# Performance work log

Measured on AMD Instinct MI355X. Metric: run time of the kernel, lower is better.

The kernel has to match this reference:

```python
import jax, jax.numpy as jnp
import numpy as np

N_NODES = 65536
N_EDGES = 524288
FEAT_DIM = 512
EMBED_DIM = 512


def setup_inputs() -> dict:
    key = jax.random.key(0)
    k1, k2, k3, k4, k5 = jax.random.split(key, 5)
    x = jax.random.normal(k1, (N_NODES, FEAT_DIM), dtype=jnp.float32)
    # xavier_uniform for (embed_dim, feat_dim)
    limit = float(np.sqrt(6.0 / (EMBED_DIM + FEAT_DIM)))
    weight = jax.random.uniform(k2, (EMBED_DIM, FEAT_DIM), dtype=jnp.float32,
                                minval=-limit, maxval=limit)
    row = jax.random.randint(k3, (N_EDGES,), 0, N_NODES, dtype=jnp.int64)
    col = jax.random.randint(k4, (N_EDGES,), 0, N_NODES, dtype=jnp.int64)
    vals = jax.random.uniform(k5, (N_EDGES,), dtype=jnp.float32)
    return {"x": x, "weight": weight, "row": row, "col": col, "vals": vals}


def reference(x, weight, row, col, vals):
    # Fused GEMM + SpMM: out = adj @ (x @ weight.T)
    h = jnp.einsum('nf,ef->ne', x, weight)            # [N, embed_dim] dense GEMM
    msgs = vals[:, None] * h[col]                     # [E, embed_dim] gather + scale
    out = jax.ops.segment_sum(msgs, row, num_segments=N_NODES)  # SpMM scatter-add
    return out
```

## Files before the change

### kernel.cpp

```cpp
#include <hip/hip_runtime.h>
#include <stdint.h>


#define N_NODES 65536
#define N_EDGES 524288
#define FEAT    512
#define EMB     512
#define CAP     64

typedef short  short8  __attribute__((ext_vector_type(8)));
typedef float  floatx4 __attribute__((ext_vector_type(4)));

__device__ __forceinline__ unsigned short f2bf(float f) {
    unsigned int u = __float_as_uint(f);
    u += 0x7FFFu + ((u >> 16) & 1u);
    return (unsigned short)(u >> 16);
}
__device__ __forceinline__ float bf2f_lo(unsigned int u) { return __uint_as_float(u << 16); }
__device__ __forceinline__ float bf2f_hi(unsigned int u) { return __uint_as_float(u & 0xffff0000u); }

#define BM 128
#define BN 64
#define BK 64
#define LDA 72

__global__ __launch_bounds__(256)
void gemm_h(const float* __restrict__ x, const float* __restrict__ w,
            unsigned short* __restrict__ h)
{
    __shared__ unsigned short As[BM][LDA];
    __shared__ unsigned short Bs[BN][LDA];

    const int t    = threadIdx.x;
    const int lane = t & 63;
    const int wave = t >> 6;
    const int wm   = wave >> 1;
    const int wn   = wave & 1;
    const int l15  = lane & 15;
    const int lq   = lane >> 4;

    const int bn = blockIdx.x & 7;
    const int bm = blockIdx.x >> 3;
    const int m0 = bm * BM;
    const int n0 = bn * BN;

    floatx4 acc[4][2];
    #pragma unroll
    for (int i = 0; i < 4; i++)
        #pragma unroll
        for (int j = 0; j < 2; j++)
            acc[i][j] = (floatx4){0.f, 0.f, 0.f, 0.f};

    for (int kb = 0; kb < FEAT; kb += BK) {
        #pragma unroll
        for (int p = 0; p < 8; p++) {
            int idx = p * 256 + t;
            int row = idx >> 4;
            int cv  = (idx & 15) << 2;
            float4 v = *(const float4*)&x[(m0 + row) * FEAT + kb + cv];
            ushort4 b4;
            b4.x = f2bf(v.x); b4.y = f2bf(v.y); b4.z = f2bf(v.z); b4.w = f2bf(v.w);
            *(ushort4*)&As[row][cv] = b4;
        }
        #pragma unroll
        for (int p = 0; p < 4; p++) {
            int idx = p * 256 + t;
            int row = idx >> 4;
            int cv  = (idx & 15) << 2;
            float4 v = *(const float4*)&w[(n0 + row) * FEAT + kb + cv];
            ushort4 b4;
            b4.x = f2bf(v.x); b4.y = f2bf(v.y); b4.z = f2bf(v.z); b4.w = f2bf(v.w);
            *(ushort4*)&Bs[row][cv] = b4;
        }
        __syncthreads();
        #pragma unroll
        for (int kk = 0; kk < 2; kk++) {
            short8 af[4], bfr[2];
            #pragma unroll
            for (int mt = 0; mt < 4; mt++)
                af[mt] = *(const short8*)&As[wm * 64 + mt * 16 + l15][kk * 32 + lq * 8];
            #pragma unroll
            for (int nt = 0; nt < 2; nt++)
                bfr[nt] = *(const short8*)&Bs[wn * 32 + nt * 16 + l15][kk * 32 + lq * 8];
            #pragma unroll
            for (int mt = 0; mt < 4; mt++)
                #pragma unroll
                for (int nt = 0; nt < 2; nt++)
                    acc[mt][nt] = __builtin_amdgcn_mfma_f32_16x16x32_bf16(
                        af[mt], bfr[nt], acc[mt][nt], 0, 0, 0);
        }
        __syncthreads();
    }

    #pragma unroll
    for (int mt = 0; mt < 4; mt++)
        #pragma unroll
        for (int nt = 0; nt < 2; nt++)
            #pragma unroll
            for (int r = 0; r < 4; r++) {
                int row  = m0 + wm * 64 + mt * 16 + lq * 4 + r;
                int colg = n0 + wn * 32 + nt * 16 + l15;
                h[row * EMB + colg] = f2bf(acc[mt][nt][r]);
            }
}

__global__ __launch_bounds__(256)
void fill_edges(const int* __restrict__ row, const int* __restrict__ col,
                const float* __restrict__ vals, int* __restrict__ cnt,
                int* __restrict__ col_s, float* __restrict__ val_s)
{
    int e = blockIdx.x * 256 + threadIdx.x;
    if (e >= N_EDGES) return;
    int r = row[e];
    int slot = atomicAdd(&cnt[r], 1);
    if (slot < CAP) {
        col_s[r * CAP + slot] = col[e];
        val_s[r * CAP + slot] = vals[e];
    }
}

__global__ __launch_bounds__(256)
void rowsum(const unsigned short* __restrict__ h, const int* __restrict__ cnt,
            const int* __restrict__ col_s, const float* __restrict__ val_s,
            float* __restrict__ out)
{
    const int r    = blockIdx.x * 4 + (threadIdx.x >> 6);
    const int lane = threadIdx.x & 63;
    int deg = cnt[r];
    if (deg > CAP) deg = CAP;

    float acc[8] = {0.f, 0.f, 0.f, 0.f, 0.f, 0.f, 0.f, 0.f};
    const int base = r * CAP;
    for (int i = 0; i < deg; i++) {
        int   c = col_s[base + i];
        float v = val_s[base + i];
        uint4 hv = *(const uint4*)&h[c * EMB + lane * 8];
        acc[0] += v * bf2f_lo(hv.x); acc[1] += v * bf2f_hi(hv.x);
        acc[2] += v * bf2f_lo(hv.y); acc[3] += v * bf2f_hi(hv.y);
        acc[4] += v * bf2f_lo(hv.z); acc[5] += v * bf2f_hi(hv.z);
        acc[6] += v * bf2f_lo(hv.w); acc[7] += v * bf2f_hi(hv.w);
    }
    float* o = &out[r * EMB + lane * 8];
    *(float4*)(o + 0) = make_float4(acc[0], acc[1], acc[2], acc[3]);
    *(float4*)(o + 4) = make_float4(acc[4], acc[5], acc[6], acc[7]);
}

__global__ __launch_bounds__(128)
void scatter_atomic(const int* __restrict__ row, const int* __restrict__ col,
                    const float* __restrict__ vals, const unsigned short* __restrict__ h,
                    float* __restrict__ out)
{
    int e = blockIdx.x;
    int r = row[e], c = col[e];
    float v = vals[e];
    int f = threadIdx.x * 4;
    uint2 hv = *(const uint2*)&h[c * EMB + f];
    float* o = &out[r * EMB + f];
    atomicAdd(o + 0, v * bf2f_lo(hv.x));
    atomicAdd(o + 1, v * bf2f_hi(hv.x));
    atomicAdd(o + 2, v * bf2f_lo(hv.y));
    atomicAdd(o + 3, v * bf2f_hi(hv.y));
}

extern "C" void kernel_launch(void* const* d_in, const int* in_sizes, int n_in,
                              void* d_out, int out_size, void* d_ws, size_t ws_size,
                              hipStream_t stream) {
    const float* x    = (const float*)d_in[0];
    const float* w    = (const float*)d_in[1];
    const int*   row  = (const int*)d_in[2];
    const int*   col  = (const int*)d_in[3];
    const float* vals = (const float*)d_in[4];
    float* out = (float*)d_out;

    char* ws = (char*)d_ws;
    unsigned short* h = (unsigned short*)ws;
    size_t off = (size_t)N_NODES * EMB * sizeof(unsigned short);
    int* cnt = (int*)(ws + off);        off += (size_t)N_NODES * 4;
    int* col_s = (int*)(ws + off);      off += (size_t)N_NODES * CAP * 4;
    float* val_s = (float*)(ws + off);  off += (size_t)N_NODES * CAP * 4;

    gemm_h<<<dim3(4096), dim3(256), 0, stream>>>(x, w, h);

    if (ws_size >= off) {
        hipMemsetAsync(cnt, 0, (size_t)N_NODES * 4, stream);
        fill_edges<<<dim3(N_EDGES / 256), dim3(256), 0, stream>>>(row, col, vals, cnt, col_s, val_s);
        rowsum<<<dim3(N_NODES / 4), dim3(256), 0, stream>>>(h, cnt, col_s, val_s, out);
    } else {
        hipMemsetAsync(out, 0, (size_t)out_size * sizeof(float), stream);
        scatter_atomic<<<dim3(N_EDGES), dim3(128), 0, stream>>>(row, col, vals, h, out);
    }
}
```

Before: 459.6 us.

## Pre-convert inputs to bf16, add LDS-direct swizzled GEMM, XCD block mapping, batched rowsum gathers

Adds kernels that convert x and the weight to bf16 ahead of time, and a new GEMM with 128x128 tiles that loads straight into LDS through global_load_lds with an XOR swizzle. Blocks are remapped so neighbouring row tiles stay on the same XCD. rowsum now loads a row's edge indices once per wave, broadcasts them with shuffles, and issues 8 gathers at a time to expose memory-level parallelism. Workspace regions are reused: the bf16 x buffer is overwritten by the edge lists after the GEMM. The price is an extra pass over x to write and reread its bf16 copy.

```diff
diff --git a/kernel.cpp b/kernel.cpp
--- a/kernel.cpp
+++ b/kernel.cpp
@@ -16,20 +16,32 @@
     u += 0x7FFFu + ((u >> 16) & 1u);
     return (unsigned short)(u >> 16);
 }
-__device__ __forceinline__ float bf2f_lo(unsigned int u) { return __uint_as_float(u << 16); }
-__device__ __forceinline__ float bf2f_hi(unsigned int u) { return __uint_as_float(u & 0xffff0000u); }
-
-#define BM 128
-#define BN 64
-#define BK 64
-#define LDA 72
-
-__global__ __launch_bounds__(256)
-void gemm_h(const float* __restrict__ x, const float* __restrict__ w,
-            unsigned short* __restrict__ h)
-{
-    __shared__ unsigned short As[BM][LDA];
-    __shared__ unsigned short Bs[BN][LDA];
+__device__ __forceinline__ float bf2f_lo(unsigned int u){ return __uint_as_float(u << 16); }
+__device__ __forceinline__ float bf2f_hi(unsigned int u){ return __uint_as_float(u & 0xffff0000u); }
+
+typedef __attribute__((address_space(1))) const void* gas_vp;
+typedef __attribute__((address_space(3))) void*       las_vp;
+#define GLDS16(g, l) __builtin_amdgcn_global_load_lds((gas_vp)(const void*)(g), (las_vp)(void*)(l), 16, 0, 0)
+
+__global__ __launch_bounds__(256)
+void conv_bf16(const float* __restrict__ in, unsigned short* __restrict__ out)
+{
+    size_t i = ((size_t)blockIdx.x * 256 + threadIdx.x) * 8;
+    float4 a = *(const float4*)&in[i];
+    float4 b = *(const float4*)&in[i + 4];
+    ushort4 lo, hi;
+    lo.x = f2bf(a.x); lo.y = f2bf(a.y); lo.z = f2bf(a.z); lo.w = f2bf(a.w);
+    hi.x = f2bf(b.x); hi.y = f2bf(b.y); hi.z = f2bf(b.z); hi.w = f2bf(b.w);
+    *(ushort4*)&out[i]     = lo;
+    *(ushort4*)&out[i + 4] = hi;
+}
+
+__global__ __launch_bounds__(256)
+void gemm_fast(const unsigned short* __restrict__ xb, const unsigned short* __restrict__ wb,
+               unsigned short* __restrict__ h)
+{
+    __shared__ unsigned short As[128 * 64];
+    __shared__ unsigned short Bs[128 * 64];
 
     const int t    = threadIdx.x;
     const int lane = t & 63;
@@ -39,68 +51,134 @@
     const int l15  = lane & 15;
     const int lq   = lane >> 4;
 
-    const int bn = blockIdx.x & 7;
-    const int bm = blockIdx.x >> 3;
-    const int m0 = bm * BM;
-    const int n0 = bn * BN;
+    const int xcd = blockIdx.x & 7;
+    const int loc = blockIdx.x >> 3;
+    const int m0  = (xcd * 64 + (loc >> 2)) * 128;
+    const int n0  = (loc & 3) * 128;
+
+    floatx4 acc[4][4];
+    #pragma unroll
+    for (int i = 0; i < 4; i++)
+        #pragma unroll
+        for (int j = 0; j < 4; j++) acc[i][j] = (floatx4){0.f, 0.f, 0.f, 0.f};
+
+    const int r8  = t >> 3;
+    const int c8  = t & 7;
+
+    for (int kb = 0; kb < FEAT; kb += 64) {
+        #pragma unroll
+        for (int p = 0; p < 4; p++) {
+            int row = p * 32 + r8;
+            int lc  = c8 ^ (row & 7);
+            GLDS16(&xb[(m0 + row) * FEAT + kb + lc * 8], &As[row * 64 + c8 * 8]);
+            GLDS16(&wb[(n0 + row) * FEAT + kb + lc * 8], &Bs[row * 64 + c8 * 8]);
+        }
+        __syncthreads();
+        #pragma unroll
+        for (int kk = 0; kk < 2; kk++) {
+            short8 af[4], bf[4];
+            #pragma unroll
+            for (int mt = 0; mt < 4; mt++) {
+                int r  = wm * 64 + mt * 16 + l15;
+                int pc = (kk * 4 + lq) ^ (r & 7);
+                af[mt] = *(const short8*)&As[r * 64 + pc * 8];
+            }
+            #pragma unroll
+            for (int nt = 0; nt < 4; nt++) {
+                int r  = wn * 64 + nt * 16 + l15;
+                int pc = (kk * 4 + lq) ^ (r & 7);
+                bf[nt] = *(const short8*)&Bs[r * 64 + pc * 8];
+            }
+            #pragma unroll
+            for (int mt = 0; mt < 4; mt++)
+                #pragma unroll
+                for (int nt = 0; nt < 4; nt++)
+                    acc[mt][nt] = __builtin_amdgcn_mfma_f32_16x16x32_bf16(
+                        af[mt], bf[nt], acc[mt][nt], 0, 0, 0);
+        }
+        __syncthreads();
+    }
+
+    #pragma unroll
+    for (int mt = 0; mt < 4; mt++)
+        #pragma unroll
+        for (int nt = 0; nt < 4; nt++)
+            #pragma unroll
+            for (int r = 0; r < 4; r++) {
+                int row = m0 + wm * 64 + mt * 16 + lq * 4 + r;
+                int col = n0 + wn * 64 + nt * 16 + l15;
+                h[row * EMB + col] = f2bf(acc[mt][nt][r]);
+            }
+}
+
+#define BM 128
+#define BN 64
+#define LDA 72
+
+__global__ __launch_bounds__(256)
+void gemm_f32(const float* __restrict__ x, const float* __restrict__ w,
+              unsigned short* __restrict__ h)
+{
+    __shared__ unsigned short As[BM][LDA];
+    __shared__ unsigned short Bs[BN][LDA];
+
+    const int t = threadIdx.x, lane = t & 63, wave = t >> 6;
+    const int wm = wave >> 1, wn = wave & 1;
+    const int l15 = lane & 15, lq = lane >> 4;
+    const int xcd = blockIdx.x & 7;
+    const int loc = blockIdx.x >> 3;
+    const int m0 = (xcd * 64 + (loc >> 3)) * BM;
+    const int n0 = (loc & 7) * BN;
 
     floatx4 acc[4][2];
     #pragma unroll
     for (int i = 0; i < 4; i++)
         #pragma unroll
-        for (int j = 0; j < 2; j++)
-            acc[i][j] = (floatx4){0.f, 0.f, 0.f, 0.f};
-
-    for (int kb = 0; kb < FEAT; kb += BK) {
+        for (int j = 0; j < 2; j++) acc[i][j] = (floatx4){0.f, 0.f, 0.f, 0.f};
+
+    for (int kb = 0; kb < FEAT; kb += 64) {
         #pragma unroll
         for (int p = 0; p < 8; p++) {
-            int idx = p * 256 + t;
-            int row = idx >> 4;
-            int cv  = (idx & 15) << 2;
+            int idx = p * 256 + t, row = idx >> 4, cv = (idx & 15) << 2;
             float4 v = *(const float4*)&x[(m0 + row) * FEAT + kb + cv];
-            ushort4 b4;
-            b4.x = f2bf(v.x); b4.y = f2bf(v.y); b4.z = f2bf(v.z); b4.w = f2bf(v.w);
+            ushort4 b4 = {f2bf(v.x), f2bf(v.y), f2bf(v.z), f2bf(v.w)};
             *(ushort4*)&As[row][cv] = b4;
         }
         #pragma unroll
         for (int p = 0; p < 4; p++) {
-            int idx = p * 256 + t;
-            int row = idx >> 4;
-            int cv  = (idx & 15) << 2;
+            int idx = p * 256 + t, row = idx >> 4, cv = (idx & 15) << 2;
             float4 v = *(const float4*)&w[(n0 + row) * FEAT + kb + cv];
-            ushort4 b4;
-            b4.x = f2bf(v.x); b4.y = f2bf(v.y); b4.z = f2bf(v.z); b4.w = f2bf(v.w);
+            ushort4 b4 = {f2bf(v.x), f2bf(v.y), f2bf(v.z), f2bf(v.w)};
             *(ushort4*)&Bs[row][cv] = b4;
         }
         __syncthreads();
         #pragma unroll
         for (int kk = 0; kk < 2; kk++) {
-            short8 af[4], bfr[2];
+            short8 af[4], bf[2];
             #pragma unroll
             for (int mt = 0; mt < 4; mt++)
                 af[mt] = *(const short8*)&As[wm * 64 + mt * 16 + l15][kk * 32 + lq * 8];
             #pragma unroll
             for (int nt = 0; nt < 2; nt++)
-                bfr[nt] = *(const short8*)&Bs[wn * 32 + nt * 16 + l15][kk * 32 + lq * 8];
+                bf[nt] = *(const short8*)&Bs[wn * 32 + nt * 16 + l15][kk * 32 + lq * 8];
             #pragma unroll
             for (int mt = 0; mt < 4; mt++)
                 #pragma unroll
                 for (int nt = 0; nt < 2; nt++)
                     acc[mt][nt] = __builtin_amdgcn_mfma_f32_16x16x32_bf16(
-                        af[mt], bfr[nt], acc[mt][nt], 0, 0, 0);
+                        af[mt], bf[nt], acc[mt][nt], 0, 0, 0);
         }
         __syncthreads();
     }
-
     #pragma unroll
     for (int mt = 0; mt < 4; mt++)
         #pragma unroll
         for (int nt = 0; nt < 2; nt++)
             #pragma unroll
             for (int r = 0; r < 4; r++) {
-                int row  = m0 + wm * 64 + mt * 16 + lq * 4 + r;
-                int colg = n0 + wn * 32 + nt * 16 + l15;
-                h[row * EMB + colg] = f2bf(acc[mt][nt][r]);
+                int row = m0 + wm * 64 + mt * 16 + lq * 4 + r;
+                int col = n0 + wn * 32 + nt * 16 + l15;
+                h[row * EMB + col] = f2bf(acc[mt][nt][r]);
             }
 }
 
@@ -128,17 +206,34 @@
     const int lane = threadIdx.x & 63;
     int deg = cnt[r];
     if (deg > CAP) deg = CAP;
-
-    float acc[8] = {0.f, 0.f, 0.f, 0.f, 0.f, 0.f, 0.f, 0.f};
     const int base = r * CAP;
-    for (int i = 0; i < deg; i++) {
-        int   c = col_s[base + i];
-        float v = val_s[base + i];
-        uint4 hv = *(const uint4*)&h[c * EMB + lane * 8];
-        acc[0] += v * bf2f_lo(hv.x); acc[1] += v * bf2f_hi(hv.x);
-        acc[2] += v * bf2f_lo(hv.y); acc[3] += v * bf2f_hi(hv.y);
-        acc[4] += v * bf2f_lo(hv.z); acc[5] += v * bf2f_hi(hv.z);
-        acc[6] += v * bf2f_lo(hv.w); acc[7] += v * bf2f_hi(hv.w);
+
+    int   c_l = 0;
+    float v_l = 0.f;
+    if (lane < deg) { c_l = col_s[base + lane]; v_l = val_s[base + lane]; }
+
+    float acc[8] = {0.f,0.f,0.f,0.f,0.f,0.f,0.f,0.f};
+    for (int i0 = 0; i0 < deg; i0 += 8) {
+        uint4 hv[8]; float vv[8];
+        int nn = deg - i0; if (nn > 8) nn = 8;
+        #pragma unroll
+        for (int j = 0; j < 8; j++) {
+            if (j < nn) {
+                int c = __shfl(c_l, i0 + j, 64);
+                vv[j] = __shfl(v_l, i0 + j, 64);
+                hv[j] = *(const uint4*)&h[c * EMB + lane * 8];
+            }
+        }
+        #pragma unroll
+        for (int j = 0; j < 8; j++) {
+            if (j < nn) {
+                float v = vv[j];
+                acc[0] += v * bf2f_lo(hv[j].x); acc[1] += v * bf2f_hi(hv[j].x);
+                acc[2] += v * bf2f_lo(hv[j].y); acc[3] += v * bf2f_hi(hv[j].y);
+                acc[4] += v * bf2f_lo(hv[j].z); acc[5] += v * bf2f_hi(hv[j].z);
+                acc[6] += v * bf2f_lo(hv[j].w); acc[7] += v * bf2f_hi(hv[j].w);
+            }
+        }
     }
     float* o = &out[r * EMB + lane * 8];
     *(float4*)(o + 0) = make_float4(acc[0], acc[1], acc[2], acc[3]);
@@ -171,21 +266,43 @@
     const int*   col  = (const int*)d_in[3];
     const float* vals = (const float*)d_in[4];
     float* out = (float*)d_out;
-
     char* ws = (char*)d_ws;
-    unsigned short* h = (unsigned short*)ws;
-    size_t off = (size_t)N_NODES * EMB * sizeof(unsigned short);
-    int* cnt = (int*)(ws + off);        off += (size_t)N_NODES * 4;
-    int* col_s = (int*)(ws + off);      off += (size_t)N_NODES * CAP * 4;
-    float* val_s = (float*)(ws + off);  off += (size_t)N_NODES * CAP * 4;
-
-    gemm_h<<<dim3(4096), dim3(256), 0, stream>>>(x, w, h);
-
-    if (ws_size >= off) {
-        hipMemsetAsync(cnt, 0, (size_t)N_NODES * 4, stream);
+
+    const size_t SZ_XB  = (size_t)N_NODES * FEAT * 2;
+    const size_t SZ_WB  = (size_t)EMB * FEAT * 2;
+    const size_t SZ_H   = (size_t)N_NODES * EMB * 2;
+    const size_t SZ_CNT = (size_t)N_NODES * 4;
+    const size_t SZ_C   = (size_t)N_NODES * CAP * 4;
+    const size_t NEED_FAST = SZ_XB + SZ_WB + SZ_H + SZ_CNT;
+    const size_t NEED_BIN  = SZ_H + SZ_CNT + 2 * SZ_C;
+
+    if (ws_size >= NEED_FAST) {
+        unsigned short* xb = (unsigned short*)ws;
+        int*   col_s = (int*)ws;
+        float* val_s = (float*)(ws + SZ_C);
+        unsigned short* wb = (unsigned short*)(ws + SZ_XB);
+        unsigned short* h  = (unsigned short*)(ws + SZ_XB + SZ_WB);
+        int* cnt = (int*)(ws + SZ_XB + SZ_WB + SZ_H);
+
+        conv_bf16<<<dim3((N_NODES * FEAT) / (256 * 8)), dim3(256), 0, stream>>>(x, xb);
+        conv_bf16<<<dim3((EMB * FEAT) / (256 * 8)), dim3(256), 0, stream>>>(w, wb);
+        gemm_fast<<<dim3(2048), dim3(256), 0, stream>>>(xb, wb, h);
+        hipMemsetAsync(cnt, 0, SZ_CNT, stream);
+        fill_edges<<<dim3(N_EDGES / 256), dim3(256), 0, stream>>>(row, col, vals, cnt, col_s, val_s);
+        rowsum<<<dim3(N_NODES / 4), dim3(256), 0, stream>>>(h, cnt, col_s, val_s, out);
+    } else if (ws_size >= NEED_BIN) {
+        unsigned short* h = (unsigned short*)ws;
+        int*   cnt   = (int*)(ws + SZ_H);
+        int*   col_s = (int*)(ws + SZ_H + SZ_CNT);
+        float* val_s = (float*)(ws + SZ_H + SZ_CNT + SZ_C);
+
+        gemm_f32<<<dim3(4096), dim3(256), 0, stream>>>(x, w, h);
+        hipMemsetAsync(cnt, 0, SZ_CNT, stream);
         fill_edges<<<dim3(N_EDGES / 256), dim3(256), 0, stream>>>(row, col, vals, cnt, col_s, val_s);
         rowsum<<<dim3(N_NODES / 4), dim3(256), 0, stream>>>(h, cnt, col_s, val_s, out);
     } else {
+        unsigned short* h = (unsigned short*)ws;
+        gemm_f32<<<dim3(4096), dim3(256), 0, stream>>>(x, w, h);
         hipMemsetAsync(out, 0, (size_t)out_size * sizeof(float), stream);
         scatter_atomic<<<dim3(N_EDGES), dim3(128), 0, stream>>>(row, col, vals, h, out);
     }
```

Measured after the change: 401.4 us. 12.6% less time.
